# Kernel tuning notes

Measured on AMD Instinct MI355X. Metric: run time of the kernel, lower is better.

Reference implementation:

```python
import jax, jax.numpy as jnp
import numpy as np

B, N, D, L = 16, 100, 1024, 2000


def setup_inputs() -> dict:
    key = jax.random.key(0)
    ks = jax.random.split(key, 9)
    s = 1.0 / np.sqrt(D)
    return {
        "feature": jax.random.normal(ks[0], (B, N, D), dtype=jnp.float32),
        "graph": jax.random.randint(ks[1], (B, N, N), 0, L),
        "W0": jax.random.normal(ks[2], (D, D), dtype=jnp.float32) * s,
        "W1": jax.random.normal(ks[3], (D, D), dtype=jnp.float32) * s,
        "bias": jax.random.uniform(ks[4], (L, D), dtype=jnp.float32, minval=-s, maxval=s),
        "dp_Wa": jax.random.normal(ks[5], (D, D), dtype=jnp.float32) * s,
        "dp_ba": jax.random.normal(ks[6], (D,), dtype=jnp.float32) * s,
        "dp_Wb": jax.random.normal(ks[7], (D, D), dtype=jnp.float32) * s,
        "dp_bb": jax.random.normal(ks[8], (D,), dtype=jnp.float32) * s,
        "get_alpha": 0,
    }


def reference(feature, graph, W0, W1, bias, dp_Wa, dp_ba, dp_Wb, dp_bb, get_alpha):
    # ---- DirectedGraphConv.conv ----
    adj = (graph != 0).astype(feature.dtype)                     # [B,N,N]
    out = feature + feature @ W0.T + feature @ W1.T              # [B,N,D]
    out = out + jnp.take(bias, graph, axis=0).sum(axis=2)        # label-embedding gather+sum over neighbors
    # ---- relation_alpha: DotProduct(feature, feature) ----
    a = feature @ dp_Wa.T + dp_ba                                # [B,N,D]
    b = feature @ dp_Wb.T + dp_bb                                # [B,N,D]
    alpha = jnp.einsum('bik,bjk->bij', a, b)                     # [B,N,N]
    alpha = jnp.maximum(alpha, 0.0)                              # alpha[alpha<0]=0
    alpha = jnp.einsum('bij,bjk->bik', adj, alpha)               # bmm(adj, alpha)
    alpha = jax.nn.softmax(alpha, axis=1)                        # Softmax(dim=1)
    out = jnp.einsum('bij,bjk->bik', alpha, out)                 # bmm(alpha, output)
    if get_alpha:
        return (out, alpha)
    return out
```

## Files before the change

kernel.cpp:

```cpp
#include <hip/hip_runtime.h>
#include <stdint.h>

#define B_   16
#define N_   100
#define D_   1024
#define L_   2000
#define M_   1600

#define RCAP 24
#define ZMAX 2400
#define TC   12

typedef __bf16 bf16x8 __attribute__((ext_vector_type(8)));
typedef float  f32x4  __attribute__((ext_vector_type(4)));

__device__ __forceinline__ void gl_lds16(const __bf16* g, __bf16* l) {
    __builtin_amdgcn_global_load_lds(
        (const __attribute__((address_space(1))) void*)g,
        (__attribute__((address_space(3))) void*)l, 16, 0, 0);
}


__global__ void __launch_bounds__(256)
k_prep(const float* __restrict__ f,
       const float* __restrict__ W0, const float* __restrict__ W1,
       const float* __restrict__ Wa, const float* __restrict__ Wb,
       const float* __restrict__ bias,
       __bf16* __restrict__ fb, __bf16* __restrict__ wcat, __bf16* __restrict__ biasB) {
    int i = blockIdx.x * 256 + threadIdx.x;
    union { __bf16 h[8]; uint4 u; } pk;
    if (i < 204800) {
        long base = (long)i * 8;
        const float4* p = (const float4*)(f + base);
        float4 x = p[0], y = p[1];
        pk.h[0]=(__bf16)x.x; pk.h[1]=(__bf16)x.y; pk.h[2]=(__bf16)x.z; pk.h[3]=(__bf16)x.w;
        pk.h[4]=(__bf16)y.x; pk.h[5]=(__bf16)y.y; pk.h[6]=(__bf16)y.z; pk.h[7]=(__bf16)y.w;
        ((uint4*)fb)[i] = pk.u;
    } else if (i < 598016) {
        int j = i - 204800;
        long base = (long)j * 8;
        long seg = base >> 20;
        long off = base & ((1l << 20) - 1);
        if (seg == 0) {
            const float4* p0 = (const float4*)(W0 + off);
            const float4* p1 = (const float4*)(W1 + off);
            float4 a0 = p0[0], a1 = p0[1], b0 = p1[0], b1 = p1[1];
            pk.h[0]=(__bf16)(a0.x+b0.x); pk.h[1]=(__bf16)(a0.y+b0.y);
            pk.h[2]=(__bf16)(a0.z+b0.z); pk.h[3]=(__bf16)(a0.w+b0.w);
            pk.h[4]=(__bf16)(a1.x+b1.x); pk.h[5]=(__bf16)(a1.y+b1.y);
            pk.h[6]=(__bf16)(a1.z+b1.z); pk.h[7]=(__bf16)(a1.w+b1.w);
        } else {
            const float* src = (seg == 1) ? Wa : Wb;
            const float4* p = (const float4*)(src + off);
            float4 x = p[0], y = p[1];
            pk.h[0]=(__bf16)x.x; pk.h[1]=(__bf16)x.y; pk.h[2]=(__bf16)x.z; pk.h[3]=(__bf16)x.w;
            pk.h[4]=(__bf16)y.x; pk.h[5]=(__bf16)y.y; pk.h[6]=(__bf16)y.z; pk.h[7]=(__bf16)y.w;
        }
        ((uint4*)wcat)[j] = pk.u;
    } else {
        int j = i - 598016;
        long base = (long)j * 8;
        const float4* p = (const float4*)(bias + base);
        float4 x = p[0], y = p[1];
        pk.h[0]=(__bf16)x.x; pk.h[1]=(__bf16)x.y; pk.h[2]=(__bf16)x.z; pk.h[3]=(__bf16)x.w;
        pk.h[4]=(__bf16)y.x; pk.h[5]=(__bf16)y.y; pk.h[6]=(__bf16)y.z; pk.h[7]=(__bf16)y.w;
        ((uint4*)biasB)[j] = pk.u;
    }
}


#define BM 64
#define BN 128
#define BK 64

__global__ void __launch_bounds__(256)
k_gemm(const __bf16* __restrict__ A, const __bf16* __restrict__ Bw,
       const float* __restrict__ feat, const float* __restrict__ ba,
       const float* __restrict__ bbias,
       float* __restrict__ out0, float* __restrict__ aB, float* __restrict__ bB) {
    __shared__ __align__(16) __bf16 As[BM * BK];
    __shared__ __align__(16) __bf16 Bs[BN * BK];
    int t = threadIdx.x;
    int bm = blockIdx.x, bn = blockIdx.y;
    int lane = t & 63, wave = t >> 6;
    int wr = wave & 1, wc = wave >> 1;
    int lrow = lane & 15, quad = lane >> 4;

    f32x4 acc[2][4] = {};
    const __bf16* Ag = A  + (long)(bm * BM) * D_;
    const __bf16* Bg = Bw + (long)(bn * BN) * D_;

    for (int k0 = 0; k0 < D_; k0 += BK) {
        #pragma unroll
        for (int pi = 0; pi < 2; ++pi) {
            int p = pi * 256 + t, row = p >> 3, c = (p & 7) ^ (row & 7);
            gl_lds16(Ag + (long)row * D_ + k0 + c * 8, As + p * 8);
        }
        #pragma unroll
        for (int pi = 0; pi < 4; ++pi) {
            int p = pi * 256 + t, row = p >> 3, c = (p & 7) ^ (row & 7);
            gl_lds16(Bg + (long)row * D_ + k0 + c * 8, Bs + p * 8);
        }
        __syncthreads();
        #pragma unroll
        for (int ks = 0; ks < 2; ++ks) {
            bf16x8 af[2], bf[4];
            #pragma unroll
            for (int i = 0; i < 2; ++i) {
                int r = wr * 32 + i * 16 + lrow;
                int slot = r * 8 + (((ks << 2) | quad) ^ (r & 7));
                af[i] = *(const bf16x8*)(As + slot * 8);
            }
            #pragma unroll
            for (int j = 0; j < 4; ++j) {
                int r = wc * 64 + j * 16 + lrow;
                int slot = r * 8 + (((ks << 2) | quad) ^ (r & 7));
                bf[j] = *(const bf16x8*)(Bs + slot * 8);
            }
            #pragma unroll
            for (int i = 0; i < 2; ++i)
                #pragma unroll
                for (int j = 0; j < 4; ++j)
                    acc[i][j] = __builtin_amdgcn_mfma_f32_16x16x32_bf16(af[i], bf[j], acc[i][j], 0, 0, 0);
        }
        __syncthreads();
    }

    int nbase = bn * BN;
    int seg = nbase >> 10;
    #pragma unroll
    for (int i = 0; i < 2; ++i) {
        int gm0 = bm * BM + wr * 32 + i * 16 + quad * 4;
        #pragma unroll
        for (int j = 0; j < 4; ++j) {
            int col = (nbase + wc * 64 + j * 16 + lrow) & 1023;
            #pragma unroll
            for (int r = 0; r < 4; ++r) {
                long m = gm0 + r;
                float v = acc[i][j][r];
                if (seg == 0)      out0[m * D_ + col] = v + feat[m * D_ + col];
                else if (seg == 1) aB[m * D_ + col]   = v + ba[col];
                else               bB[m * D_ + col]   = v + bbias[col];
            }
        }
    }
}


__global__ void __launch_bounds__(256)
k_ga(const int* __restrict__ graph, const __bf16* __restrict__ biasB,
     float* __restrict__ out0, const float* __restrict__ aB,
     const float* __restrict__ bB, float* __restrict__ wl, float* __restrict__ cwG) {
    __shared__ int rowCnt[N_], rowOff[N_], rowRank[N_];
    __shared__ int ndvS, totZS;
    __shared__ int zjL[ZMAX];
    __shared__ short prL[ZMAX];
    __shared__ float corrL[RCAP][4];
    __shared__ float wred[4][4];

    int t = threadIdx.x;
    if (blockIdx.x < 1600) {
        int bi = blockIdx.x;
        if (t < N_) rowCnt[t] = graph[(long)bi * N_ + t];
        __syncthreads();
        float a0 = 0.f, a1 = 0.f, a2 = 0.f, a3 = 0.f;
        #pragma unroll 4
        for (int j = 0; j < N_; ++j) {
            int lb = rowCnt[j];
            union { uint2 u; __bf16 h[4]; } pk;
            pk.u = ((const uint2*)(biasB + (long)lb * D_))[t];
            a0 += (float)pk.h[0]; a1 += (float)pk.h[1];
            a2 += (float)pk.h[2]; a3 += (float)pk.h[3];
        }
        float4* o = (float4*)(out0 + (long)bi * D_) + t;
        float4 cur = *o;
        cur.x += a0; cur.y += a1; cur.z += a2; cur.w += a3;
        *o = cur;
        return;
    }

    int pid = blockIdx.x - 1600;
    int b = pid / 25, kc = pid - b * 25;
    int lane = t & 63, wave = t >> 6;

    const int* g = graph + (long)b * N_ * N_;
    if (t < N_) {
        int c = 0;
        for (int j = 0; j < N_; ++j) if (g[t * N_ + j] == 0) ++c;
        rowCnt[t] = c;
    }
    if (t < RCAP * 4) corrL[t >> 2][t & 3] = 0.f;
    __syncthreads();
    if (t == 0) {
        int off = 0, rank = 0;
        for (int i = 0; i < N_; ++i) {
            if (rowCnt[i] > 0 && rank < RCAP) {
                rowRank[i] = rank; rowOff[i] = off; off += rowCnt[i]; ++rank;
            } else rowRank[i] = -1;
        }
        ndvS = rank; totZS = off;
    }
    __syncthreads();
    if (t < N_ && rowRank[t] >= 0) {
        int pos = rowOff[t], r = rowRank[t];
        for (int j = 0; j < N_; ++j)
            if (g[t * N_ + j] == 0) { zjL[pos] = j; prL[pos] = (short)r; ++pos; }
    }
    __syncthreads();
    int Z = totZS, ndv = ndvS;

    int k0 = kc * 4;
    float4 bv[4];
    #pragma unroll
    for (int kk = 0; kk < 4; ++kk)
        bv[kk] = *(const float4*)(bB + ((long)(b * N_ + k0 + kk)) * D_ + t * 4);

    for (int q = 0; q < Z; ++q) {
        const float* ar = aB + ((long)(b * N_ + zjL[q])) * D_;
        float4 av = *(const float4*)(ar + t * 4);
        float s[4];
        #pragma unroll
        for (int kk = 0; kk < 4; ++kk)
            s[kk] = av.x * bv[kk].x + av.y * bv[kk].y + av.z * bv[kk].z + av.w * bv[kk].w;
        #pragma unroll
        for (int off = 32; off > 0; off >>= 1)
            #pragma unroll
            for (int kk = 0; kk < 4; ++kk) s[kk] += __shfl_xor(s[kk], off);
        if (lane == 0) { wred[wave][0]=s[0]; wred[wave][1]=s[1]; wred[wave][2]=s[2]; wred[wave][3]=s[3]; }
        __syncthreads();
        if (t < 4) {
            float v = wred[0][t] + wred[1][t] + wred[2][t] + wred[3][t];
            corrL[prL[q]][t] += fmaxf(v, 0.f);
        }
        __syncthreads();
    }

    if (t < 4) {
        int k = k0 + t;
        float denom = (float)(N_ - ndv);
        for (int r = 0; r < ndv; ++r) {
            float e = __expf(-corrL[r][t]);
            corrL[r][t] = e;
            denom += e;
        }
        float w = 1.f / denom;
        wl[b * N_ + k] = w;
        for (int r = 0; r < ndv; ++r)
            cwG[((long)b * RCAP + r) * N_ + k] = corrL[r][t] * w;
    }
}


__global__ void __launch_bounds__(256)
k_mix(const int* __restrict__ graph, const float* __restrict__ wl,
      const float* __restrict__ cwG, const float* __restrict__ out0,
      float* __restrict__ out) {
    int b = blockIdx.x, dq = blockIdx.y;
    int t = threadIdx.x, c = t & 127, h = t >> 7;
    int d0 = dq * 128;
    __shared__ int hasZ[N_], mapL[N_], ndvS;
    __shared__ float wT[TC][N_];
    __shared__ float parts[2][TC][128];

    const int* g = graph + (long)b * N_ * N_;
    if (t < N_) {
        int z = 0;
        for (int j = 0; j < N_; ++j) if (g[t * N_ + j] == 0) { z = 1; break; }
        hasZ[t] = z;
    }
    __syncthreads();
    if (t < N_) {
        int rank = 0;
        for (int i = 0; i < t; ++i) rank += hasZ[i];
        mapL[t] = (hasZ[t] && rank < RCAP) ? 1 + rank : 0;
    }
    if (t == 0) {
        int n = 0;
        for (int i = 0; i < N_; ++i) n += hasZ[i];
        ndvS = min(n, RCAP);
    }
    __syncthreads();
    int ndv = ndvS, ntask = ndv + 1;

    const float* o0 = out0 + (long)b * N_ * D_ + d0;
    for (int cb = 0; cb < ntask; cb += TC) {
        for (int idx = t; idx < TC * N_; idx += 256) {
            int rr = idx / N_, j = idx - rr * N_;
            int task = cb + rr;
            float v = 0.f;
            if (task == 0)         v = wl[b * N_ + j];
            else if (task <= ndv)  v = cwG[((long)b * RCAP + task - 1) * N_ + j];
            wT[rr][j] = v;
        }
        __syncthreads();
        float acc[TC] = {};
        #pragma unroll 2
        for (int j = h * 50; j < h * 50 + 50; ++j) {
            float v = o0[(long)j * D_ + c];
            #pragma unroll
            for (int rr = 0; rr < TC; ++rr) acc[rr] += wT[rr][j] * v;
        }
        #pragma unroll
        for (int rr = 0; rr < TC; ++rr) parts[h][rr][c] = acc[rr];
        __syncthreads();
        for (int i = h * 50; i < h * 50 + 50; ++i) {
            int task = mapL[i];
            if (task >= cb && task < cb + TC) {
                int rr = task - cb;
                out[((long)(b * N_ + i)) * D_ + d0 + c] = parts[0][rr][c] + parts[1][rr][c];
            }
        }
        __syncthreads();
    }
}


extern "C" void kernel_launch(void* const* d_in, const int* in_sizes, int n_in,
                              void* d_out, int out_size, void* d_ws, size_t ws_size,
                              hipStream_t stream) {
    const float* feature = (const float*)d_in[0];
    const int*   graph   = (const int*)d_in[1];
    const float* W0      = (const float*)d_in[2];
    const float* W1      = (const float*)d_in[3];
    const float* bias    = (const float*)d_in[4];
    const float* dp_Wa   = (const float*)d_in[5];
    const float* dp_ba   = (const float*)d_in[6];
    const float* dp_Wb   = (const float*)d_in[7];
    const float* dp_bb   = (const float*)d_in[8];
    float* out = (float*)d_out;

    char* w = (char*)d_ws;
    __bf16* fb16  = (__bf16*)(w);
    __bf16* wcat  = (__bf16*)(w + 3276800);
    __bf16* biasB = (__bf16*)(w + 9568256);
    float*  out0  = (float*)(w + 13664256);
    float*  aB    = (float*)(w + 20217856);
    float*  bB    = (float*)(w + 26771456);
    float*  wl    = (float*)(w + 33325056);
    float*  cwG   = (float*)(w + 33331456);

    k_prep<<<3336, 256, 0, stream>>>(feature, W0, W1, dp_Wa, dp_Wb, bias,
                                     fb16, wcat, biasB);
    k_gemm<<<dim3(25, 24), 256, 0, stream>>>(fb16, wcat, feature, dp_ba, dp_bb,
                                             out0, aB, bB);
    k_ga<<<2000, 256, 0, stream>>>(graph, biasB, out0, aB, bB, wl, cwG);
    k_mix<<<dim3(B_, 8), 256, 0, stream>>>(graph, wl, cwG, out0, out);
}
```

Baseline: 186.0 us.

## Remap GEMM blocks for L2 locality, tile bias gather by rows, vectorize mix

Measured after the change: 177.8 us. -4.4%, faster.

```diff
diff --git a/kernel.cpp b/kernel.cpp
--- a/kernel.cpp
+++ b/kernel.cpp
@@ -74,22 +74,24 @@
 #define BK 64
 
 __global__ void __launch_bounds__(256)
-k_gemm(const __bf16* __restrict__ A, const __bf16* __restrict__ Bw,
+k_gemm(const __bf16* __restrict__ fb, const __bf16* __restrict__ wcat,
        const float* __restrict__ feat, const float* __restrict__ ba,
        const float* __restrict__ bbias,
        float* __restrict__ out0, float* __restrict__ aB, float* __restrict__ bB) {
     __shared__ __align__(16) __bf16 As[BM * BK];
     __shared__ __align__(16) __bf16 Bs[BN * BK];
     int t = threadIdx.x;
-    int bm = blockIdx.x, bn = blockIdx.y;
+    int pid = blockIdx.x;
     int lane = t & 63, wave = t >> 6;
     int wr = wave & 1, wc = wave >> 1;
     int lrow = lane & 15, quad = lane >> 4;
 
+    int v = (pid & 7) * 75 + (pid >> 3);
+    int bn = v / 25, bm = v % 25;
+    const __bf16* Ag = fb   + (long)(bm * BM) * D_;
+    const __bf16* Bg = wcat + (long)(bn * BN) * D_;
+
     f32x4 acc[2][4] = {};
-    const __bf16* Ag = A  + (long)(bm * BM) * D_;
-    const __bf16* Bg = Bw + (long)(bn * BN) * D_;
-
     for (int k0 = 0; k0 < D_; k0 += BK) {
         #pragma unroll
         for (int pi = 0; pi < 2; ++pi) {
@@ -127,7 +129,7 @@
     }
 
     int nbase = bn * BN;
-    int seg = nbase >> 10;
+    int seg = bn >> 3;
     #pragma unroll
     for (int i = 0; i < 2; ++i) {
         int gm0 = bm * BM + wr * 32 + i * 16 + quad * 4;
@@ -137,10 +139,10 @@
             #pragma unroll
             for (int r = 0; r < 4; ++r) {
                 long m = gm0 + r;
-                float v = acc[i][j][r];
-                if (seg == 0)      out0[m * D_ + col] = v + feat[m * D_ + col];
-                else if (seg == 1) aB[m * D_ + col]   = v + ba[col];
-                else               bB[m * D_ + col]   = v + bbias[col];
+                float v2 = acc[i][j][r];
+                if (seg == 0)      out0[m * D_ + col] = v2 + feat[m * D_ + col];
+                else if (seg == 1) aB[m * D_ + col]   = v2 + ba[col];
+                else               bB[m * D_ + col]   = v2 + bbias[col];
             }
         }
     }
@@ -148,9 +150,9 @@
 
 
 __global__ void __launch_bounds__(256)
-k_ga(const int* __restrict__ graph, const __bf16* __restrict__ biasB,
-     float* __restrict__ out0, const float* __restrict__ aB,
-     const float* __restrict__ bB, float* __restrict__ wl, float* __restrict__ cwG) {
+k_ga(const int* __restrict__ graph, const float* __restrict__ aB,
+     const float* __restrict__ bB, const __bf16* __restrict__ biasB,
+     float* __restrict__ out0, float* __restrict__ wl, float* __restrict__ cwG) {
     __shared__ int rowCnt[N_], rowOff[N_], rowRank[N_];
     __shared__ int ndvS, totZS;
     __shared__ int zjL[ZMAX];
@@ -158,28 +160,34 @@
     __shared__ float corrL[RCAP][4];
     __shared__ float wred[4][4];
 
-    int t = threadIdx.x;
-    if (blockIdx.x < 1600) {
-        int bi = blockIdx.x;
-        if (t < N_) rowCnt[t] = graph[(long)bi * N_ + t];
-        __syncthreads();
+    int pid = blockIdx.x, t = threadIdx.x;
+
+    if (pid >= 400) {
+        int gp = pid - 400;
+        int ds = gp & 7, rg = gp >> 3;
+        int r = t >> 5, cp = t & 31;
+        for (int idx = t; idx < 800; idx += 256)
+            zjL[idx] = graph[(long)(rg * 8 + idx / 100) * N_ + idx % 100];
+        __syncthreads();
+        const __bf16* bp = biasB + ds * 128 + cp * 4;
+        const int* my = zjL + r * 100;
         float a0 = 0.f, a1 = 0.f, a2 = 0.f, a3 = 0.f;
         #pragma unroll 4
         for (int j = 0; j < N_; ++j) {
-            int lb = rowCnt[j];
+            int lb = my[j];
             union { uint2 u; __bf16 h[4]; } pk;
-            pk.u = ((const uint2*)(biasB + (long)lb * D_))[t];
+            pk.u = *(const uint2*)(bp + (long)lb * D_);
             a0 += (float)pk.h[0]; a1 += (float)pk.h[1];
             a2 += (float)pk.h[2]; a3 += (float)pk.h[3];
         }
-        float4* o = (float4*)(out0 + (long)bi * D_) + t;
+        long bi = rg * 8 + r;
+        float4* o = (float4*)(out0 + bi * D_ + ds * 128 + cp * 4);
         float4 cur = *o;
         cur.x += a0; cur.y += a1; cur.z += a2; cur.w += a3;
         *o = cur;
         return;
     }
 
-    int pid = blockIdx.x - 1600;
     int b = pid / 25, kc = pid - b * 25;
     int lane = t & 63, wave = t >> 6;
 
@@ -256,11 +264,11 @@
       const float* __restrict__ cwG, const float* __restrict__ out0,
       float* __restrict__ out) {
     int b = blockIdx.x, dq = blockIdx.y;
-    int t = threadIdx.x, c = t & 127, h = t >> 7;
-    int d0 = dq * 128;
+    int t = threadIdx.x, c4 = t & 63, q = t >> 6;
+    int d0 = dq * 256;
     __shared__ int hasZ[N_], mapL[N_], ndvS;
     __shared__ float wT[TC][N_];
-    __shared__ float parts[2][TC][128];
+    __shared__ f32x4 parts[4][TC][64];
 
     const int* g = graph + (long)b * N_ * N_;
     if (t < N_) {
@@ -293,21 +301,22 @@
             wT[rr][j] = v;
         }
         __syncthreads();
-        float acc[TC] = {};
-        #pragma unroll 2
-        for (int j = h * 50; j < h * 50 + 50; ++j) {
-            float v = o0[(long)j * D_ + c];
+        f32x4 acc[TC] = {};
+        for (int j = q * 25; j < q * 25 + 25; ++j) {
+            f32x4 v = *(const f32x4*)(o0 + (long)j * D_ + c4 * 4);
             #pragma unroll
             for (int rr = 0; rr < TC; ++rr) acc[rr] += wT[rr][j] * v;
         }
         #pragma unroll
-        for (int rr = 0; rr < TC; ++rr) parts[h][rr][c] = acc[rr];
-        __syncthreads();
-        for (int i = h * 50; i < h * 50 + 50; ++i) {
+        for (int rr = 0; rr < TC; ++rr) parts[q][rr][c4] = acc[rr];
+        __syncthreads();
+        for (int i = q * 25; i < q * 25 + 25; ++i) {
             int task = mapL[i];
             if (task >= cb && task < cb + TC) {
                 int rr = task - cb;
-                out[((long)(b * N_ + i)) * D_ + d0 + c] = parts[0][rr][c] + parts[1][rr][c];
+                f32x4 s = parts[0][rr][c4] + parts[1][rr][c4]
+                        + parts[2][rr][c4] + parts[3][rr][c4];
+                *(f32x4*)(out + ((long)(b * N_ + i)) * D_ + d0 + c4 * 4) = s;
             }
         }
         __syncthreads();
@@ -341,8 +350,8 @@
 
     k_prep<<<3336, 256, 0, stream>>>(feature, W0, W1, dp_Wa, dp_Wb, bias,
                                      fb16, wcat, biasB);
-    k_gemm<<<dim3(25, 24), 256, 0, stream>>>(fb16, wcat, feature, dp_ba, dp_bb,
-                                             out0, aB, bB);
-    k_ga<<<2000, 256, 0, stream>>>(graph, biasB, out0, aB, bB, wl, cwG);
-    k_mix<<<dim3(B_, 8), 256, 0, stream>>>(graph, wl, cwG, out0, out);
-}
+    k_gemm<<<600, 256, 0, stream>>>(fb16, wcat, feature, dp_ba, dp_bb,
+                                    out0, aB, bB);
+    k_ga<<<2000, 256, 0, stream>>>(graph, aB, bB, biasB, out0, wl, cwG);
+    k_mix<<<dim3(B_, 4), 256, 0, stream>>>(graph, wl, cwG, out0, out);
+}
```
